# Optimization experiments

Measured on AMD Instinct MI355X. Metric: run time of the kernel, lower is better.

## Reference

```python
import jax, jax.numpy as jnp
import numpy as np

DIM = 1024
HEADS = 16
DIM_HEAD = 64
INNER = HEADS * DIM_HEAD  # 1024
SCALE = DIM_HEAD ** -0.5


def setup_inputs() -> dict:
    key = jax.random.key(0)
    k0, k1, k2 = jax.random.split(key, 3)
    x = jax.random.normal(k0, (4, 2048, DIM), dtype=jnp.float32)
    ln_gamma = jnp.ones((DIM,), dtype=jnp.float32)
    ln_beta = jnp.zeros((DIM,), dtype=jnp.float32)
    w_qkv = jax.random.normal(k1, (DIM, 3 * INNER), dtype=jnp.float32) * (DIM ** -0.5)
    w_out = jax.random.normal(k2, (INNER, DIM), dtype=jnp.float32) * (INNER ** -0.5)
    b_out = jnp.zeros((DIM,), dtype=jnp.float32)
    return {"x": x, "ln_gamma": ln_gamma, "ln_beta": ln_beta,
            "w_qkv": w_qkv, "w_out": w_out, "b_out": b_out}


def reference(x, ln_gamma, ln_beta, w_qkv, w_out, b_out):
    # LayerNorm over last dim (eps matches torch default 1e-5)
    mu = jnp.mean(x, axis=-1, keepdims=True)
    var = jnp.mean(jnp.square(x - mu), axis=-1, keepdims=True)
    xn = (x - mu) * jax.lax.rsqrt(var + 1e-5) * ln_gamma + ln_beta
    # QKV projection (no bias)
    qkv = xn @ w_qkv  # [b, t, 3*inner]
    q, k, v = jnp.split(qkv, 3, axis=-1)
    B, T, _ = x.shape
    def to_heads(t):
        return t.reshape(B, T, HEADS, DIM_HEAD).transpose(0, 2, 1, 3)  # b h t d
    q, k, v = to_heads(q), to_heads(k), to_heads(v)
    dots = jnp.einsum('bhid,bhjd->bhij', q, k) * SCALE
    attn = jax.nn.softmax(dots, axis=-1)
    out = jnp.einsum('bhij,bhjd->bhid', attn, v)
    out = out.transpose(0, 2, 1, 3).reshape(B, T, INNER)
    return out @ w_out + b_out
```

## Files before the change

kernel.cpp:

```cpp
#include <hip/hip_runtime.h>


#define DIMX 1024
#define TSEQ 2048
#define NB 4
#define NH 16
#define DH 64
#define NROWS (NB * TSEQ)
#define QSCALE 0.18033688011112042f

typedef __bf16 bf16_t;
typedef __bf16 bf16x8 __attribute__((ext_vector_type(8)));
typedef __bf16 bf16x4 __attribute__((ext_vector_type(4)));
typedef float f32x4 __attribute__((ext_vector_type(4)));

#if __has_builtin(__builtin_amdgcn_exp2f)
#define EXP2F __builtin_amdgcn_exp2f
#else
#define EXP2F exp2f
#endif

__device__ __forceinline__ bf16x4 cvt4(f32x4 v) {
    return __builtin_convertvector(v, bf16x4);
}
__device__ __forceinline__ void async16(const bf16_t* g, bf16_t* l) {
    __builtin_amdgcn_global_load_lds(
        (const __attribute__((address_space(1))) unsigned int*)g,
        (__attribute__((address_space(3))) unsigned int*)l, 16, 0, 0);
}

__global__ __launch_bounds__(256) void ln_kernel(
    const float* __restrict__ x, const float* __restrict__ g,
    const float* __restrict__ b, bf16_t* __restrict__ xn) {
    int row = blockIdx.x, tid = threadIdx.x;
    const float4 xv = *(const float4*)(x + (size_t)row * DIMX + tid * 4);
    float s = xv.x + xv.y + xv.z + xv.w;
    float q = xv.x * xv.x + xv.y * xv.y + xv.z * xv.z + xv.w * xv.w;
    for (int o = 32; o > 0; o >>= 1) {
        s += __shfl_xor(s, o);
        q += __shfl_xor(q, o);
    }
    __shared__ float2 red[4];
    int wave = tid >> 6, lane = tid & 63;
    if (lane == 0) red[wave] = make_float2(s, q);
    __syncthreads();
    float2 r0 = red[0], r1 = red[1], r2 = red[2], r3 = red[3];
    s = r0.x + r1.x + r2.x + r3.x;
    q = r0.y + r1.y + r2.y + r3.y;
    float mu = s * (1.0f / DIMX);
    float var = q * (1.0f / DIMX) - mu * mu;
    float rstd = rsqrtf(var + 1e-5f);
    float4 gv = *(const float4*)(g + tid * 4);
    float4 bv = *(const float4*)(b + tid * 4);
    f32x4 r;
    r[0] = (xv.x - mu) * rstd * gv.x + bv.x;
    r[1] = (xv.y - mu) * rstd * gv.y + bv.y;
    r[2] = (xv.z - mu) * rstd * gv.z + bv.z;
    r[3] = (xv.w - mu) * rstd * gv.w + bv.w;
    *(bf16x4*)(xn + (size_t)row * DIMX + tid * 4) = cvt4(r);
}

__global__ __launch_bounds__(256) void transpose_cast(
    const float* __restrict__ src, bf16_t* __restrict__ dst, int R, int C) {
    __shared__ float tile[32][33];
    int c0 = blockIdx.x * 32, r0 = blockIdx.y * 32;
    int tx = threadIdx.x, ty = threadIdx.y;
    for (int i = ty; i < 32; i += 8)
        tile[i][tx] = src[(size_t)(r0 + i) * C + c0 + tx];
    __syncthreads();
    for (int i = ty; i < 32; i += 8)
        dst[(size_t)(c0 + i) * R + r0 + tx] = (bf16_t)tile[tx][i];
}

template <int MODE>
__global__ __launch_bounds__(256) void gemm128(
    const bf16_t* __restrict__ A, const bf16_t* __restrict__ BT,
    void* __restrict__ Cout, const float* __restrict__ bias, int M, int N, int K) {
    __shared__ __align__(16) bf16_t As[128 * 32];
    __shared__ __align__(16) bf16_t Bs[128 * 32];
    int tid = threadIdx.x, lane = tid & 63, wave = tid >> 6;
    int lm = lane & 15, quad = lane >> 4;
    int wr = wave >> 1, wc = wave & 1;
    int n0 = blockIdx.x * 128, m0 = blockIdx.y * 128;
    const bf16_t* ga = A + (size_t)(m0 + (tid >> 2)) * K + (tid & 3) * 8;
    const bf16_t* gb = BT + (size_t)(n0 + (tid >> 2)) * K + (tid & 3) * 8;
    bf16_t* la = &As[tid * 8];
    bf16_t* lb = &Bs[tid * 8];
    f32x4 zero = {0.f, 0.f, 0.f, 0.f};
    f32x4 acc[4][4];
#pragma unroll
    for (int i = 0; i < 4; ++i)
#pragma unroll
        for (int j = 0; j < 4; ++j) acc[i][j] = zero;

    for (int k0 = 0; k0 < K; k0 += 32) {
        __syncthreads();
        async16(ga + k0, la);
        async16(ga + (size_t)64 * K + k0, la + 2048);
        async16(gb + k0, lb);
        async16(gb + (size_t)64 * K + k0, lb + 2048);
        __syncthreads();
        bf16x8 af[4], bf[4];
#pragma unroll
        for (int t = 0; t < 4; ++t) {
            af[t] = *(const bf16x8*)&As[(wr * 64 + t * 16 + lm) * 32 + quad * 8];
            bf[t] = *(const bf16x8*)&Bs[(wc * 64 + t * 16 + lm) * 32 + quad * 8];
        }
#pragma unroll
        for (int mt = 0; mt < 4; ++mt)
#pragma unroll
            for (int nt = 0; nt < 4; ++nt)
                acc[mt][nt] = __builtin_amdgcn_mfma_f32_16x16x32_bf16(af[mt], bf[nt], acc[mt][nt], 0, 0, 0);
    }

#pragma unroll
    for (int mt = 0; mt < 4; ++mt) {
#pragma unroll
        for (int nt = 0; nt < 4; ++nt) {
            int m = m0 + wr * 64 + mt * 16 + quad * 4;
            int n = n0 + wc * 64 + nt * 16 + lm;
            if (MODE == 1) {
                int sel = n >> 10, nn = n & 1023, h = nn >> 6, d = nn & 63;
                int b = m >> 11, t = m & 2047;
                if (sel == 2) {
                    *(bf16x4*)((bf16_t*)Cout + (size_t)2 * 8388608 +
                               ((size_t)((b * NH + h) * DH + d)) * TSEQ + t) = cvt4(acc[mt][nt]);
                } else {
                    f32x4 sv = acc[mt][nt] * (sel == 0 ? QSCALE : 1.0f);
                    bf16x4 c4 = cvt4(sv);
#pragma unroll
                    for (int r = 0; r < 4; ++r)
                        ((bf16_t*)Cout)[(size_t)sel * 8388608 +
                                        ((size_t)((b * NH + h) * TSEQ + t + r)) * DH + d] = c4[r];
                }
            } else {
                float bn = bias[n];
#pragma unroll
                for (int r = 0; r < 4; ++r)
                    ((float*)Cout)[(size_t)(m + r) * N + n] = acc[mt][nt][r] + bn;
            }
        }
    }
}

__global__ __launch_bounds__(256, 2) void attn_mfma(
    const bf16_t* __restrict__ qkv, bf16_t* __restrict__ o) {
    int bh = blockIdx.y;
    int qt = blockIdx.x;
    const bf16_t* qb = qkv + (size_t)bh * TSEQ * DH;
    const bf16_t* kb = qkv + (size_t)8388608 + (size_t)bh * TSEQ * DH;
    const bf16_t* vb = qkv + (size_t)16777216 + (size_t)bh * DH * TSEQ;
    int tid = threadIdx.x, wave = tid >> 6, lane = tid & 63;
    int lm = lane & 15, quad = lane >> 4, lx = lm & 7;

    __shared__ __align__(16) bf16_t Ks[64 * 64];
    __shared__ __align__(16) bf16_t Vt[64 * 64];
    __shared__ __align__(16) bf16_t Ps[4 * 1024];

    int roff = tid >> 3;
    int cperm = ((tid & 7) ^ (roff & 7)) * 8;
    const bf16_t* kp0 = kb + (size_t)roff * DH + cperm;
    const bf16_t* kp1 = kb + (size_t)(32 + roff) * DH + cperm;
    const bf16_t* vp0 = vb + (size_t)roff * TSEQ + cperm;
    const bf16_t* vp1 = vb + (size_t)(32 + roff) * TSEQ + cperm;
    bf16_t* lk0 = &Ks[tid * 8];
    bf16_t* lk1 = &Ks[(256 + tid) * 8];
    bf16_t* lv0 = &Vt[tid * 8];
    bf16_t* lv1 = &Vt[(256 + tid) * 8];

    bf16x8 qf[4][2];
#pragma unroll
    for (int u = 0; u < 4; ++u)
#pragma unroll
        for (int ks = 0; ks < 2; ++ks)
            qf[u][ks] = *(const bf16x8*)(qb +
                (size_t)(qt * 256 + wave * 64 + u * 16 + lm) * DH + ks * 32 + quad * 8);

    f32x4 zero = {0.f, 0.f, 0.f, 0.f};
    f32x4 m16 = {-16.f, -16.f, -16.f, -16.f};
    f32x4 acc[4][4];
#pragma unroll
    for (int u = 0; u < 4; ++u)
#pragma unroll
        for (int dt = 0; dt < 4; ++dt) acc[u][dt] = zero;
    f32x4 l4[4] = {zero, zero, zero, zero};

    int fo0 = (quad ^ lx) * 8;
    int fo1 = ((4 + quad) ^ lx) * 8;
    int pb = wave * 1024 + lm * 64;

    for (int jt = 0; jt < TSEQ / 64; ++jt) {
        __syncthreads();
        async16(kp0, lk0);
        async16(kp1, lk1);
        async16(vp0, lv0);
        async16(vp1, lv1);
        kp0 += 64 * DH; kp1 += 64 * DH; vp0 += 64; vp1 += 64;
        __syncthreads();

        bf16x8 kf[4][2];
#pragma unroll
        for (int nt = 0; nt < 4; ++nt) {
            kf[nt][0] = *(const bf16x8*)&Ks[(nt * 16 + lm) * 64 + fo0];
            kf[nt][1] = *(const bf16x8*)&Ks[(nt * 16 + lm) * 64 + fo1];
        }

        bf16x8 pf[4][2];
#pragma unroll
        for (int u = 0; u < 4; ++u) {
            f32x4 s[4];
#pragma unroll
            for (int nt = 0; nt < 4; ++nt) {
                s[nt] = __builtin_amdgcn_mfma_f32_16x16x32_bf16(kf[nt][0], qf[u][0], m16, 0, 0, 0);
                s[nt] = __builtin_amdgcn_mfma_f32_16x16x32_bf16(kf[nt][1], qf[u][1], s[nt], 0, 0, 0);
            }
#pragma unroll
            for (int nt = 0; nt < 4; ++nt) {
                f32x4 p;
#pragma unroll
                for (int e = 0; e < 4; ++e) p[e] = EXP2F(s[nt][e]);
                l4[u] += p;
                *(bf16x4*)&Ps[pb + ((nt * 2 + (quad >> 1)) ^ lx) * 8 + (quad & 1) * 4] = cvt4(p);
            }
            pf[u][0] = *(const bf16x8*)&Ps[pb + fo0];
            pf[u][1] = *(const bf16x8*)&Ps[pb + fo1];
        }

#pragma unroll
        for (int dt = 0; dt < 4; ++dt) {
            bf16x8 vf0 = *(const bf16x8*)&Vt[(dt * 16 + lm) * 64 + fo0];
            bf16x8 vf1 = *(const bf16x8*)&Vt[(dt * 16 + lm) * 64 + fo1];
#pragma unroll
            for (int u = 0; u < 4; ++u) {
                acc[u][dt] = __builtin_amdgcn_mfma_f32_16x16x32_bf16(vf0, pf[u][0], acc[u][dt], 0, 0, 0);
                acc[u][dt] = __builtin_amdgcn_mfma_f32_16x16x32_bf16(vf1, pf[u][1], acc[u][dt], 0, 0, 0);
            }
        }
    }

    int b = bh >> 4, h = bh & 15;
#pragma unroll
    for (int u = 0; u < 4; ++u) {
        float l = (l4[u][0] + l4[u][1]) + (l4[u][2] + l4[u][3]);
        l += __shfl_xor(l, 16);
        l += __shfl_xor(l, 32);
        float rl = 1.0f / l;
        int t = qt * 256 + wave * 64 + u * 16 + lm;
#pragma unroll
        for (int dt = 0; dt < 4; ++dt) {
            f32x4 ov = acc[u][dt] * rl;
            *(bf16x4*)(o + ((size_t)(b * TSEQ + t)) * DIMX + h * DH + dt * 16 + quad * 4) = cvt4(ov);
        }
    }
}

extern "C" void kernel_launch(void* const* d_in, const int* in_sizes, int n_in,
                              void* d_out, int out_size, void* d_ws, size_t ws_size,
                              hipStream_t stream) {
    const float* x = (const float*)d_in[0];
    const float* g = (const float*)d_in[1];
    const float* be = (const float*)d_in[2];
    const float* w_qkv = (const float*)d_in[3];
    const float* w_out = (const float*)d_in[4];
    const float* b_out = (const float*)d_in[5];
    float* out = (float*)d_out;
    char* ws = (char*)d_ws;

    bf16_t* xn = (bf16_t*)(ws);
    bf16_t* wqkvT = (bf16_t*)(ws + 16777216);
    bf16_t* woutT = (bf16_t*)(ws + 23068672);
    bf16_t* qkv = (bf16_t*)(ws + 25165824);
    bf16_t* attno = (bf16_t*)(ws + 75497472);

    ln_kernel<<<NROWS, 256, 0, stream>>>(x, g, be, xn);
    transpose_cast<<<dim3(96, 32), dim3(32, 8), 0, stream>>>(w_qkv, wqkvT, 1024, 3072);
    transpose_cast<<<dim3(32, 32), dim3(32, 8), 0, stream>>>(w_out, woutT, 1024, 1024);
    gemm128<1><<<dim3(24, 64), 256, 0, stream>>>(xn, wqkvT, (void*)qkv, nullptr, NROWS, 3072, 1024);
    attn_mfma<<<dim3(8, 64), 256, 0, stream>>>(qkv, attno);
    gemm128<2><<<dim3(8, 64), 256, 0, stream>>>(attno, woutT, (void*)out, b_out, NROWS, 1024, 1024);
}
```

Before: 289.1 us.

## Rewrite GEMM as 256x256 double-buffered, swizzled-LDS tile with XCD-aware block remap

```diff
diff --git a/kernel.cpp b/kernel.cpp
--- a/kernel.cpp
+++ b/kernel.cpp
@@ -72,52 +72,159 @@
         dst[(size_t)(c0 + i) * R + r0 + tx] = (bf16_t)tile[tx][i];
 }
 
+#define MFMA16 __builtin_amdgcn_mfma_f32_16x16x32_bf16
+
 template <int MODE>
-__global__ __launch_bounds__(256) void gemm128(
+__global__ __launch_bounds__(512, 2) void gemm256(
     const bf16_t* __restrict__ A, const bf16_t* __restrict__ BT,
     void* __restrict__ Cout, const float* __restrict__ bias, int M, int N, int K) {
-    __shared__ __align__(16) bf16_t As[128 * 32];
-    __shared__ __align__(16) bf16_t Bs[128 * 32];
+    __shared__ __align__(16) bf16_t As[2][256 * 64];
+    __shared__ __align__(16) bf16_t Bs[2][256 * 64];
     int tid = threadIdx.x, lane = tid & 63, wave = tid >> 6;
     int lm = lane & 15, quad = lane >> 4;
-    int wr = wave >> 1, wc = wave & 1;
-    int n0 = blockIdx.x * 128, m0 = blockIdx.y * 128;
-    const bf16_t* ga = A + (size_t)(m0 + (tid >> 2)) * K + (tid & 3) * 8;
-    const bf16_t* gb = BT + (size_t)(n0 + (tid >> 2)) * K + (tid & 3) * 8;
-    bf16_t* la = &As[tid * 8];
-    bf16_t* lb = &Bs[tid * 8];
+    int wr = wave >> 2, wc = wave & 3;
+
+    int nbx = gridDim.x;
+    int nwg = nbx * gridDim.y;
+    int linear = blockIdx.y * nbx + blockIdx.x;
+    int cpx = nwg >> 3;
+    int swz = (linear & 7) * cpx + (linear >> 3);
+    int bx = swz % nbx, by = swz / nbx;
+    int m0 = by * 256, n0 = bx * 256;
+
+    int srow = tid >> 3, sc8 = tid & 7;
+    int scol = (sc8 ^ (srow & 7)) << 3;
+    const bf16_t* ga = A + (size_t)(m0 + srow) * K + scol;
+    const bf16_t* gb = BT + (size_t)(n0 + srow) * K + scol;
+    int ldst = tid << 3;
+
+    int sw0 = ((quad ^ (lm & 7)) << 3);
+    int sw1 = (((4 + quad) ^ (lm & 7)) << 3);
+
     f32x4 zero = {0.f, 0.f, 0.f, 0.f};
-    f32x4 acc[4][4];
-#pragma unroll
-    for (int i = 0; i < 4; ++i)
+    f32x4 acc[8][4];
+#pragma unroll
+    for (int i = 0; i < 8; ++i)
 #pragma unroll
         for (int j = 0; j < 4; ++j) acc[i][j] = zero;
 
-    for (int k0 = 0; k0 < K; k0 += 32) {
-        __syncthreads();
-        async16(ga + k0, la);
-        async16(ga + (size_t)64 * K + k0, la + 2048);
-        async16(gb + k0, lb);
-        async16(gb + (size_t)64 * K + k0, lb + 2048);
-        __syncthreads();
-        bf16x8 af[4], bf[4];
+#pragma unroll
+    for (int i = 0; i < 4; ++i) async16(ga + (size_t)i * 64 * K, &As[0][i * 4096 + ldst]);
+#pragma unroll
+    for (int i = 0; i < 4; ++i) async16(gb + (size_t)i * 64 * K, &Bs[0][i * 4096 + ldst]);
+    asm volatile("s_waitcnt vmcnt(0)" ::: "memory");
+    __builtin_amdgcn_s_barrier();
+
+    int nkt = K >> 6;
+    for (int kt = 0; kt < nkt; ++kt) {
+        int c = kt & 1;
+        int k1 = (kt + 1) << 6;
+        bool pf = (kt + 1) < nkt;
+        const bf16_t* pa = &As[c][0];
+        const bf16_t* pb = &Bs[c][0];
+        bf16_t* na = &As[c ^ 1][0];
+        bf16_t* nb = &Bs[c ^ 1][0];
+        bf16x8 af[4][2], bfr[2][2];
+
 #pragma unroll
         for (int t = 0; t < 4; ++t) {
-            af[t] = *(const bf16x8*)&As[(wr * 64 + t * 16 + lm) * 32 + quad * 8];
-            bf[t] = *(const bf16x8*)&Bs[(wc * 64 + t * 16 + lm) * 32 + quad * 8];
-        }
+            int ro = (wr * 128 + t * 16 + lm) * 64;
+            af[t][0] = *(const bf16x8*)&pa[ro + sw0];
+            af[t][1] = *(const bf16x8*)&pa[ro + sw1];
+        }
+#pragma unroll
+        for (int t = 0; t < 2; ++t) {
+            int ro = (wc * 64 + t * 16 + lm) * 64;
+            bfr[t][0] = *(const bf16x8*)&pb[ro + sw0];
+            bfr[t][1] = *(const bf16x8*)&pb[ro + sw1];
+        }
+        if (pf) {
+#pragma unroll
+            for (int i = 0; i < 4; ++i)
+                async16(ga + (size_t)i * 64 * K + k1, &na[i * 4096 + ldst]);
+        }
+        __builtin_amdgcn_s_barrier();
+        asm volatile("s_waitcnt lgkmcnt(0)" ::: "memory");
+        __builtin_amdgcn_s_setprio(1);
 #pragma unroll
         for (int mt = 0; mt < 4; ++mt)
 #pragma unroll
-            for (int nt = 0; nt < 4; ++nt)
-                acc[mt][nt] = __builtin_amdgcn_mfma_f32_16x16x32_bf16(af[mt], bf[nt], acc[mt][nt], 0, 0, 0);
-    }
-
-#pragma unroll
-    for (int mt = 0; mt < 4; ++mt) {
+            for (int nt = 0; nt < 2; ++nt) {
+                acc[mt][nt] = MFMA16(af[mt][0], bfr[nt][0], acc[mt][nt], 0, 0, 0);
+                acc[mt][nt] = MFMA16(af[mt][1], bfr[nt][1], acc[mt][nt], 0, 0, 0);
+            }
+        __builtin_amdgcn_s_setprio(0);
+        __builtin_amdgcn_s_barrier();
+
+#pragma unroll
+        for (int t = 0; t < 2; ++t) {
+            int ro = (wc * 64 + (2 + t) * 16 + lm) * 64;
+            bfr[t][0] = *(const bf16x8*)&pb[ro + sw0];
+            bfr[t][1] = *(const bf16x8*)&pb[ro + sw1];
+        }
+        if (pf) {
+#pragma unroll
+            for (int i = 0; i < 4; ++i)
+                async16(gb + (size_t)i * 64 * K + k1, &nb[i * 4096 + ldst]);
+        }
+        __builtin_amdgcn_s_barrier();
+        asm volatile("s_waitcnt lgkmcnt(0)" ::: "memory");
+        __builtin_amdgcn_s_setprio(1);
+#pragma unroll
+        for (int mt = 0; mt < 4; ++mt)
+#pragma unroll
+            for (int nt = 0; nt < 2; ++nt) {
+                acc[mt][2 + nt] = MFMA16(af[mt][0], bfr[nt][0], acc[mt][2 + nt], 0, 0, 0);
+                acc[mt][2 + nt] = MFMA16(af[mt][1], bfr[nt][1], acc[mt][2 + nt], 0, 0, 0);
+            }
+        __builtin_amdgcn_s_setprio(0);
+        __builtin_amdgcn_s_barrier();
+
+#pragma unroll
+        for (int t = 0; t < 4; ++t) {
+            int ro = (wr * 128 + (4 + t) * 16 + lm) * 64;
+            af[t][0] = *(const bf16x8*)&pa[ro + sw0];
+            af[t][1] = *(const bf16x8*)&pa[ro + sw1];
+        }
+        __builtin_amdgcn_s_barrier();
+        asm volatile("s_waitcnt lgkmcnt(0)" ::: "memory");
+        __builtin_amdgcn_s_setprio(1);
+#pragma unroll
+        for (int mt = 0; mt < 4; ++mt)
+#pragma unroll
+            for (int nt = 0; nt < 2; ++nt) {
+                acc[4 + mt][2 + nt] = MFMA16(af[mt][0], bfr[nt][0], acc[4 + mt][2 + nt], 0, 0, 0);
+                acc[4 + mt][2 + nt] = MFMA16(af[mt][1], bfr[nt][1], acc[4 + mt][2 + nt], 0, 0, 0);
+            }
+        __builtin_amdgcn_s_setprio(0);
+        __builtin_amdgcn_s_barrier();
+
+#pragma unroll
+        for (int t = 0; t < 2; ++t) {
+            int ro = (wc * 64 + t * 16 + lm) * 64;
+            bfr[t][0] = *(const bf16x8*)&pb[ro + sw0];
+            bfr[t][1] = *(const bf16x8*)&pb[ro + sw1];
+        }
+        __builtin_amdgcn_s_barrier();
+        asm volatile("s_waitcnt lgkmcnt(0)" ::: "memory");
+        __builtin_amdgcn_s_setprio(1);
+#pragma unroll
+        for (int mt = 0; mt < 4; ++mt)
+#pragma unroll
+            for (int nt = 0; nt < 2; ++nt) {
+                acc[4 + mt][nt] = MFMA16(af[mt][0], bfr[nt][0], acc[4 + mt][nt], 0, 0, 0);
+                acc[4 + mt][nt] = MFMA16(af[mt][1], bfr[nt][1], acc[4 + mt][nt], 0, 0, 0);
+            }
+        __builtin_amdgcn_s_setprio(0);
+        asm volatile("s_waitcnt vmcnt(0)" ::: "memory");
+        __builtin_amdgcn_s_barrier();
+    }
+
+#pragma unroll
+    for (int mt = 0; mt < 8; ++mt) {
 #pragma unroll
         for (int nt = 0; nt < 4; ++nt) {
-            int m = m0 + wr * 64 + mt * 16 + quad * 4;
+            int m = m0 + wr * 128 + mt * 16 + quad * 4;
             int n = n0 + wc * 64 + nt * 16 + lm;
             if (MODE == 1) {
                 int sel = n >> 10, nn = n & 1023, h = nn >> 6, d = nn & 63;
@@ -275,7 +382,7 @@
     ln_kernel<<<NROWS, 256, 0, stream>>>(x, g, be, xn);
     transpose_cast<<<dim3(96, 32), dim3(32, 8), 0, stream>>>(w_qkv, wqkvT, 1024, 3072);
     transpose_cast<<<dim3(32, 32), dim3(32, 8), 0, stream>>>(w_out, woutT, 1024, 1024);
-    gemm128<1><<<dim3(24, 64), 256, 0, stream>>>(xn, wqkvT, (void*)qkv, nullptr, NROWS, 3072, 1024);
+    gemm256<1><<<dim3(12, 32), 512, 0, stream>>>(xn, wqkvT, (void*)qkv, nullptr, NROWS, 3072, 1024);
     attn_mfma<<<dim3(8, 64), 256, 0, stream>>>(qkv, attno);
-    gemm128<2><<<dim3(8, 64), 256, 0, stream>>>(attno, woutT, (void*)out, b_out, NROWS, 1024, 1024);
-}
+    gemm256<2><<<dim3(4, 32), 512, 0, stream>>>(attno, woutT, (void*)out, b_out, NROWS, 1024, 1024);
+}
```

Result: no change. 287.3 us (-0.6%).
